# Kernel optimization log

Hardware: AMD Instinct MI355X
Metric: run time of the kernel (lower is better)

The kernel has to match this reference:

```python
import jax, jax.numpy as jnp
import numpy as np
from jax.scipy.special import logsumexp

PAD, SOS, EOS = 0, 2, 3
V, E, H, L, K = 30000, 128, 256, 2, 32   # vocab, embed, hidden, lstm layers, tags
B, T = 64, 512
HP = H // L                               # per-direction hidden size (PyTorch: hidden_sz//num_layer)


def setup_inputs() -> dict:
    key = jax.random.key(0)
    ks = jax.random.split(key, 20)
    # sorted-descending lengths (pack_padded_sequence requirement)
    lengths = jnp.sort(jax.random.randint(ks[0], (B,), T // 2, T + 1))[::-1]
    pos = jnp.arange(T)
    valid = pos[None, :] < lengths[:, None]
    x = jnp.where(valid, jax.random.randint(ks[1], (B, T), 4, V), PAD)
    y = jax.random.randint(ks[2], (B, T + 1), 4, K).at[:, 0].set(SOS)
    embed = jax.random.normal(ks[3], (V, E)) * 0.1
    s = 1.0 / np.sqrt(HP)
    u = lambda k, shape: jax.random.uniform(k, shape, minval=-s, maxval=s)
    p = {}
    i = 4
    for l, din in [(0, E), (1, 2 * HP)]:
        for d in 'fb':
            p['wi_l%d%s' % (l, d)] = u(ks[i], (4 * HP, din)); i += 1
            p['wh_l%d%s' % (l, d)] = u(ks[i], (4 * HP, HP)); i += 1
            p['b_l%d%s' % (l, d)] = u(ks[i], (4 * HP,)); i += 1
    so = 1.0 / np.sqrt(H)
    w_out = jax.random.uniform(ks[i], (K, H), minval=-so, maxval=so); i += 1
    b_out = jax.random.uniform(ks[i], (K,), minval=-so, maxval=so); i += 1
    trans = jax.random.normal(ks[i], (K, K))
    trans = trans.at[SOS, :].set(-10000.0)
    trans = trans.at[:, EOS].set(-10000.0)
    trans = trans.at[:, PAD].set(-10000.0)
    trans = trans.at[PAD, :].set(-10000.0)
    trans = trans.at[PAD, EOS].set(0.0)
    trans = trans.at[PAD, PAD].set(0.0)
    return {'x': x, 'y': y, 'embed': embed, **p, 'w_out': w_out, 'b_out': b_out, 'trans': trans}


def _lstm_dir(xs, wi, wh, b):
    # xs: [T, B, D] -> hidden states [T, B, HP]; PyTorch gate order i, f, g, o
    bsz = xs.shape[1]
    def step(carry, xt):
        h, c = carry
        z = xt @ wi.T + h @ wh.T + b
        i, f, g, o = jnp.split(z, 4, axis=-1)
        c = jax.nn.sigmoid(f) * c + jax.nn.sigmoid(i) * jnp.tanh(g)
        h = jax.nn.sigmoid(o) * jnp.tanh(c)
        return (h, c), h
    init = (jnp.zeros((bsz, HP), xs.dtype), jnp.zeros((bsz, HP), xs.dtype))
    _, hs = jax.lax.scan(step, init, xs)
    return hs


def _flip(a, lengths):
    # per-sequence reversal of valid prefix (matches packed-sequence reverse LSTM)
    pos = jnp.arange(a.shape[1])
    idx = jnp.where(pos[None, :] < lengths[:, None], lengths[:, None] - 1 - pos[None, :], pos[None, :])
    return jnp.take_along_axis(a, idx[:, :, None], axis=1)


def _bilstm_layer(inp, lengths, wif, whf, bf, wib, whb, bb):
    hf = _lstm_dir(inp.swapaxes(0, 1), wif, whf, bf).swapaxes(0, 1)
    hb = _flip(_lstm_dir(_flip(inp, lengths).swapaxes(0, 1), wib, whb, bb).swapaxes(0, 1), lengths)
    return jnp.concatenate([hf, hb], axis=-1)


def _forward(x, y, embed, wi_l0f, wh_l0f, b_l0f, wi_l0b, wh_l0b, b_l0b,
             wi_l1f, wh_l1f, b_l1f, wi_l1b, wh_l1b, b_l1b, w_out, b_out, trans):
    mask = (x > PAD).astype(jnp.float32)          # [B, T]
    lengths = mask.sum(1).astype(jnp.int32)       # [B]
    h = embed[x]                                  # [B, T, E]
    h = _bilstm_layer(h, lengths, wi_l0f, wh_l0f, b_l0f, wi_l0b, wh_l0b, b_l0b)
    h = _bilstm_layer(h, lengths, wi_l1f, wh_l1f, b_l1f, wi_l1b, wh_l1b, b_l1b)
    h = jnp.einsum('btd,kd->btk', h, w_out) + b_out   # emissions [B, T, K]
    h = h * mask[:, :, None]
    bsz = x.shape[0]
    # CRF partition function: sequential log-sum-exp recurrence
    init = jnp.full((bsz, K), -10000.0).at[:, SOS].set(0.0)
    def step(score, tb):
        h_t, m_t = tb                              # [B, K], [B]
        s = logsumexp(score[:, None, :] + h_t[:, :, None] + trans[None, :, :], axis=-1)
        return jnp.where(m_t[:, None] > 0, s, score), None
    score, _ = jax.lax.scan(step, init, (h.swapaxes(0, 1), mask.T))
    logZ = logsumexp(score + trans[EOS], axis=-1)
    # gold path score
    emit = jnp.take_along_axis(h, y[:, 1:, None], axis=2)[..., 0]  # [B, T]
    tr = trans[y[:, 1:], y[:, :-1]]                                 # [B, T]
    gold = ((emit + tr) * mask).sum(1)
    last_tag = jnp.take_along_axis(y, lengths[:, None], axis=1)[:, 0]
    gold = gold + trans[EOS, last_tag]
    return logZ - gold                              # [B] negative log-likelihood


def reference(x, y, embed, wi_l0f, wh_l0f, b_l0f, wi_l0b, wh_l0b, b_l0b,
              wi_l1f, wh_l1f, b_l1f, wi_l1b, wh_l1b, b_l1b, w_out, b_out, trans):
    return _forward(x, y, embed, wi_l0f, wh_l0f, b_l0f, wi_l0b, wh_l0b, b_l0b,
                    wi_l1f, wh_l1f, b_l1f, wi_l1b, wh_l1b, b_l1b, w_out, b_out, trans)
```

## Files before the change

### kernel.cpp

```cpp
#include <hip/hip_runtime.h>

typedef _Float16 half_t;
typedef _Float16 half2_t __attribute__((ext_vector_type(2)));
typedef _Float16 half4_t __attribute__((ext_vector_type(4)));
typedef _Float16 half8_t __attribute__((ext_vector_type(8)));
typedef float float4_t __attribute__((ext_vector_type(4)));

#define BB 64
#define TT 512
#define EE 128
#define HPP 128
#define KK 32
#define MTOT (BB*TT)
#define NWID 1024

__device__ __forceinline__ void lds_barrier() {
    asm volatile("s_waitcnt lgkmcnt(0)\n\ts_barrier" ::: "memory");
}

__device__ __forceinline__ float fast_sigmoid(float x) {
    return __builtin_amdgcn_rcpf(1.f + __expf(-x));
}
__device__ __forceinline__ float fast_tanh(float x) {
    return 1.f - 2.f * __builtin_amdgcn_rcpf(__expf(2.f * x) + 1.f);
}
__device__ __forceinline__ float readlane_f(float v, int lane) {
    return __builtin_bit_cast(float, __builtin_amdgcn_readlane(__builtin_bit_cast(int, v), lane));
}

__global__ void k_pack(const float* __restrict__ wi0f, const float* __restrict__ wi0b,
                       const float* __restrict__ wi1f, const float* __restrict__ wi1b,
                       const float* __restrict__ w_out,
                       const int* __restrict__ x, const float* __restrict__ embed,
                       half_t* __restrict__ WP0, half_t* __restrict__ WP1,
                       half_t* __restrict__ WO, half_t* __restrict__ e16,
                       int* __restrict__ lens) {
    if (blockIdx.x < BB) {
        __shared__ int cnt;
        if (threadIdx.x == 0) cnt = 0;
        __syncthreads();
        int local = 0;
        for (int t = threadIdx.x; t < TT; t += blockDim.x)
            local += (x[blockIdx.x * TT + t] > 0) ? 1 : 0;
        atomicAdd(&cnt, local);
        __syncthreads();
        if (threadIdx.x == 0) lens[blockIdx.x] = cnt;
    }

    int idx = blockIdx.x * blockDim.x + threadIdx.x;
    int stride = gridDim.x * blockDim.x;
    const int n0 = NWID * EE;
    const int n1 = NWID * 256;
    for (int i = idx; i < n0; i += stride) {
        int j8 = i & 7; int ln = (i >> 3) & 63; int rest = i >> 9;
        int kc = rest & 3; int ntg = rest >> 2;
        int lr = ln & 15, lq = ln >> 4;
        int n = ntg * 16 + lr;
        int k = kc * 32 + lq * 8 + j8;
        float v = (n < 512) ? wi0f[n * 128 + k] : wi0b[(n - 512) * 128 + k];
        WP0[i] = (half_t)v;
    }
    for (int i = idx; i < n1; i += stride) {
        int j8 = i & 7; int ln = (i >> 3) & 63; int rest = i >> 9;
        int kc = rest & 7; int ntg = rest >> 3;
        int lr = ln & 15, lq = ln >> 4;
        int n = ntg * 16 + lr;
        int k = kc * 32 + lq * 8 + j8;
        float v = (n < 512) ? wi1f[n * 256 + k] : wi1b[(n - 512) * 256 + k];
        WP1[i] = (half_t)v;
    }
    for (int i = idx; i < KK * 256; i += stride)
        WO[i] = (half_t)w_out[i];
    for (int i = idx; i < MTOT * 16; i += stride) {
        int bt = i >> 4;
        int c  = (i & 15) * 8;
        int xi = x[bt];
        const float4* src = (const float4*)(embed + (size_t)xi * EE + c);
        float4 a = src[0], b = src[1];
        half8_t o;
        o[0] = (half_t)a.x; o[1] = (half_t)a.y; o[2] = (half_t)a.z; o[3] = (half_t)a.w;
        o[4] = (half_t)b.x; o[5] = (half_t)b.y; o[6] = (half_t)b.z; o[7] = (half_t)b.w;
        *(half8_t*)(e16 + (size_t)bt * EE + c) = o;
    }
}

__global__ __launch_bounds__(256, 2) void k_gemm(const half_t* __restrict__ A,
                                                 const half_t* __restrict__ WP,
                                                 const float* __restrict__ bias_f,
                                                 const float* __restrict__ bias_b,
                                                 const int* __restrict__ lens,
                                                 half_t* __restrict__ C, int Kd) {
    {
        int t0 = (blockIdx.x * 128) & 511;
        if (t0 >= lens[blockIdx.x >> 2]) return;
    }
    const int KC = Kd >> 5;
    int wave = threadIdx.x >> 6;
    int lane = threadIdx.x & 63;
    int m0 = blockIdx.x * 128 + wave * 32;
    int dir = blockIdx.y >> 1;
    int cg  = blockIdx.y & 1;
    int lr = lane & 15;
    int lq = lane >> 4;

    float4_t acc0[16], acc1[16];
    #pragma unroll
    for (int i = 0; i < 16; i++) {
        acc0[i] = (float4_t){0.f, 0.f, 0.f, 0.f};
        acc1[i] = (float4_t){0.f, 0.f, 0.f, 0.f};
    }

    const half_t* Arow0 = A + (size_t)(m0 + lr) * Kd + lq * 8;
    const half_t* Arow1 = Arow0 + (size_t)16 * Kd;
    const int ntile0 = dir * 32 + cg * 4;
    const half_t* Wbase = WP + ((size_t)ntile0 * KC * 64 + lane) * 8;

    for (int kc = 0; kc < KC; kc++) {
        half8_t af0 = *(const half8_t*)(Arow0 + kc * 32);
        half8_t af1 = *(const half8_t*)(Arow1 + kc * 32);
        #pragma unroll
        for (int nt = 0; nt < 16; nt++) {
            int g = nt >> 2, sub = nt & 3;
            half8_t bf = *(const half8_t*)(Wbase + (((size_t)(g * 8 + sub) * KC + kc) << 9));
            acc0[nt] = __builtin_amdgcn_mfma_f32_16x16x32_f16(af0, bf, acc0[nt], 0, 0, 0);
            acc1[nt] = __builtin_amdgcn_mfma_f32_16x16x32_f16(af1, bf, acc1[nt], 0, 0, 0);
        }
    }

    const float* bias = dir ? bias_b : bias_f;
    char* Crow = (char*)C + dir * 1024 + (size_t)(cg * 64) * 8;
    #pragma unroll
    for (int sub = 0; sub < 4; sub++) {
        int cbase = cg * 64 + sub * 16 + lr;
        float b0 = bias[cbase];
        float b1 = bias[128 + cbase];
        float b2 = bias[256 + cbase];
        float b3 = bias[384 + cbase];
        #pragma unroll
        for (int i = 0; i < 4; i++) {
            int m = m0 + lq * 4 + i;
            half4_t o;
            o[0] = (half_t)(acc0[0 * 4 + sub][i] + b0);
            o[1] = (half_t)(acc0[1 * 4 + sub][i] + b1);
            o[2] = (half_t)(acc0[2 * 4 + sub][i] + b2);
            o[3] = (half_t)(acc0[3 * 4 + sub][i] + b3);
            *(half4_t*)(Crow + (size_t)m * 2048 + (sub * 16 + lr) * 8) = o;
            half4_t o2;
            o2[0] = (half_t)(acc1[0 * 4 + sub][i] + b0);
            o2[1] = (half_t)(acc1[1 * 4 + sub][i] + b1);
            o2[2] = (half_t)(acc1[2 * 4 + sub][i] + b2);
            o2[3] = (half_t)(acc1[3 * 4 + sub][i] + b3);
            *(half4_t*)(Crow + (size_t)(m + 16) * 2048 + (sub * 16 + lr) * 8) = o2;
        }
    }
}

__global__ __launch_bounds__(512, 1) void k_lstm(const half_t* __restrict__ zbuf,
                                                 const float* __restrict__ wh_f,
                                                 const float* __restrict__ wh_b,
                                                 const int* __restrict__ lens,
                                                 half_t* __restrict__ hout) {
    const int grp  = blockIdx.x >> 1;
    const int dir  = blockIdx.x & 1;
    const int tid  = threadIdx.x;
    const int wv   = tid >> 6;
    const int lane = tid & 63;
    const int q    = lane >> 4;
    const int col  = lane & 15;
    const int s    = col & 3;
    const int ii   = col >> 2;
    const int b    = grp * 4 + s;
    const int Lb   = lens[b];
    const int maxL = lens[grp * 4];
    const float* wh = dir ? wh_b : wh_f;

    __shared__ half_t hb[2][512];

    half8_t a0[4], a1[4], a2[4], a3[4];
    #pragma unroll
    for (int i = 0; i < 4; i++) {
        int r = wv * 64 + i * 16 + col;
        int orow = (r & 3) * 128 + (r >> 2);
        #pragma unroll
        for (int ck = 0; ck < 4; ck++) {
            const float4* src = (const float4*)(wh + (size_t)orow * 128 + ck * 32 + q * 8);
            float4 f0 = src[0], f1 = src[1];
            half8_t h8;
            h8[0] = (half_t)f0.x; h8[1] = (half_t)f0.y; h8[2] = (half_t)f0.z; h8[3] = (half_t)f0.w;
            h8[4] = (half_t)f1.x; h8[5] = (half_t)f1.y; h8[6] = (half_t)f1.z; h8[7] = (half_t)f1.w;
            if (i == 0) a0[ck] = h8;
            else if (i == 1) a1[ck] = h8;
            else if (i == 2) a2[ck] = h8;
            else a3[ck] = h8;
        }
    }

    hb[0][tid] = (half_t)0.f;

    const int cell = wv * 16 + ii * 4 + q;
    const int woff = (cell >> 5) * 128 + (s * 4 + ((cell >> 3) & 3)) * 8 + (cell & 7);
    const int roff = (s * 4 + q) * 8;

    const bool s1 = (ii == 1), s2 = (ii == 2), s3 = (ii == 3);

    float c = 0.f;
    const char* zb8  = (const char*)zbuf + dir * 1024;
    char*       hob8 = (char*)hout + dir * 256;

    const int zdelta = dir ? -2048 : 2048;
    const int hdelta = dir ? -512 : 512;

    int t0 = dir ? (Lb - 1) : 0;
    int t1 = dir ? (Lb - 2) : 1;
    half4_t z1 = *(const half4_t*)(zb8 + (unsigned)((b * TT + t0) * 2048 + cell * 8));
    half4_t z2 = *(const half4_t*)(zb8 + (unsigned)((b * TT + t1) * 2048 + cell * 8));

    int zoff = (b * TT + (dir ? (Lb - 3) : 2)) * 2048 + cell * 8;
    int hoff = (b * TT + t0) * 512 + cell * 2;
    const unsigned deadoff = (unsigned)((b * TT + 511) * 512 + cell * 2);

    __syncthreads();

    const int maxL2 = (maxL + 1) & ~1;

#define LSTM_STEP(RB, ZC, T)                                                      \
    {                                                                             \
        half8_t bf0 = *(const half8_t*)&hb[RB][roff];                             \
        half8_t bf1 = *(const half8_t*)&hb[RB][128 + roff];                       \
        half8_t bf2 = *(const half8_t*)&hb[RB][256 + roff];                       \
        half8_t bf3 = *(const half8_t*)&hb[RB][384 + roff];                       \
        float4_t A0 = (float4_t){0.f, 0.f, 0.f, 0.f};                             \
        float4_t A1 = (float4_t){0.f, 0.f, 0.f, 0.f};                             \
        float4_t A2 = (float4_t){0.f, 0.f, 0.f, 0.f};                             \
        float4_t A3 = (float4_t){0.f, 0.f, 0.f, 0.f};                             \
        A0 = __builtin_amdgcn_mfma_f32_16x16x32_f16(a0[0], bf0, A0, 0, 0, 0);     \
        A1 = __builtin_amdgcn_mfma_f32_16x16x32_f16(a1[0], bf0, A1, 0, 0, 0);     \
        A2 = __builtin_amdgcn_mfma_f32_16x16x32_f16(a2[0], bf0, A2, 0, 0, 0);     \
        A3 = __builtin_amdgcn_mfma_f32_16x16x32_f16(a3[0], bf0, A3, 0, 0, 0);     \
        A0 = __builtin_amdgcn_mfma_f32_16x16x32_f16(a0[1], bf1, A0, 0, 0, 0);     \
        A1 = __builtin_amdgcn_mfma_f32_16x16x32_f16(a1[1], bf1, A1, 0, 0, 0);     \
        A2 = __builtin_amdgcn_mfma_f32_16x16x32_f16(a2[1], bf1, A2, 0, 0, 0);     \
        A3 = __builtin_amdgcn_mfma_f32_16x16x32_f16(a3[1], bf1, A3, 0, 0, 0);     \
        A0 = __builtin_amdgcn_mfma_f32_16x16x32_f16(a0[2], bf2, A0, 0, 0, 0);     \
        A1 = __builtin_amdgcn_mfma_f32_16x16x32_f16(a1[2], bf2, A1, 0, 0, 0);     \
        A2 = __builtin_amdgcn_mfma_f32_16x16x32_f16(a2[2], bf2, A2, 0, 0, 0);     \
        A3 = __builtin_amdgcn_mfma_f32_16x16x32_f16(a3[2], bf2, A3, 0, 0, 0);     \
        A0 = __builtin_amdgcn_mfma_f32_16x16x32_f16(a0[3], bf3, A0, 0, 0, 0);     \
        A1 = __builtin_amdgcn_mfma_f32_16x16x32_f16(a1[3], bf3, A1, 0, 0, 0);     \
        A2 = __builtin_amdgcn_mfma_f32_16x16x32_f16(a2[3], bf3, A2, 0, 0, 0);     \
        A3 = __builtin_amdgcn_mfma_f32_16x16x32_f16(a3[3], bf3, A3, 0, 0, 0);     \
        float g0 = s1 ? A1[0] : (s2 ? A2[0] : (s3 ? A3[0] : A0[0]));              \
        float g1 = s1 ? A1[1] : (s2 ? A2[1] : (s3 ? A3[1] : A0[1]));              \
        float g2 = s1 ? A1[2] : (s2 ? A2[2] : (s3 ? A3[2] : A0[2]));              \
        float g3 = s1 ? A1[3] : (s2 ? A2[3] : (s3 ? A3[3] : A0[3]));              \
        float zi = g0 + (float)ZC[0];                                             \
        float zf = g1 + (float)ZC[1];                                             \
        float zg = g2 + (float)ZC[2];                                             \
        float zo = g3 + (float)ZC[3];                                             \
        ZC = *(const half4_t*)(zb8 + (unsigned)zoff);         \
        zoff += zdelta;                                                           \
        zoff = zoff < 0 ? 0 : zoff;                                               \
        float si = fast_sigmoid(zi);                                              \
        float sf = fast_sigmoid(zf);                                              \
        float so = fast_sigmoid(zo);                                              \
        float tg = fast_tanh(zg);                                                 \
        c = sf * c + si * tg;                                                     \
        float th = fast_tanh(c);                                                  \
        half_t hh = (half_t)(so * th);                                            \
        hb[RB ^ 1][woff] = hh;                                                    \
        unsigned soff = ((T) < Lb) ? (unsigned)hoff : deadoff;                    \
        *(half_t*)(hob8 + soff) = hh;                        \
        hoff += hdelta;                                                           \
        lds_barrier();                                                            \
    }

    for (int t = 0; t < maxL2; t += 2) {
        LSTM_STEP(0, z1, t)
        LSTM_STEP(1, z2, t + 1)
    }
#undef LSTM_STEP
}

__global__ __launch_bounds__(256) void k_logits(const half_t* __restrict__ h1,
                                                const half_t* __restrict__ WO,
                                                const float* __restrict__ b_out,
                                                const int* __restrict__ lens,
                                                float* __restrict__ logits) {
    {
        int t0 = (blockIdx.x * 64) & 511;
        if (t0 >= lens[blockIdx.x >> 3]) return;
    }
    int wave = threadIdx.x >> 6;
    int lane = threadIdx.x & 63;
    int m0 = blockIdx.x * 64 + wave * 16;
    int lr = lane & 15;
    int lq = lane >> 4;

    float4_t acc0 = (float4_t){0.f, 0.f, 0.f, 0.f};
    float4_t acc1 = (float4_t){0.f, 0.f, 0.f, 0.f};

    const half_t* Arow = h1 + (size_t)(m0 + lr) * 256 + lq * 8;
    const half_t* Brow = WO + (size_t)lr * 256 + lq * 8;

    #pragma unroll
    for (int k = 0; k < 256; k += 32) {
        half8_t af = *(const half8_t*)(Arow + k);
        half8_t b0 = *(const half8_t*)(Brow + k);
        half8_t b1 = *(const half8_t*)(Brow + 16 * 256 + k);
        acc0 = __builtin_amdgcn_mfma_f32_16x16x32_f16(af, b0, acc0, 0, 0, 0);
        acc1 = __builtin_amdgcn_mfma_f32_16x16x32_f16(af, b1, acc1, 0, 0, 0);
    }
    #pragma unroll
    for (int nt = 0; nt < 2; nt++) {
        int n = nt * 16 + lr;
        float bias = b_out[n];
        #pragma unroll
        for (int i = 0; i < 4; i++) {
            int m = m0 + lq * 4 + i;
            logits[(size_t)m * KK + n] = (nt == 0 ? acc0[i] : acc1[i]) + bias;
        }
    }
}

__global__ __launch_bounds__(64) void k_crf(const float* __restrict__ logits,
                                            const float* __restrict__ trans,
                                            const int* __restrict__ y,
                                            const int* __restrict__ lens,
                                            float* __restrict__ out) {
    int b = blockIdx.x;
    int lane = threadIdx.x;
    int k = lane & 31;
    __shared__ float TR[32][33];

    for (int i = lane; i < 1024; i += 64) TR[i >> 5][i & 31] = trans[i];

    float et[32];
    const float* trow = trans + k * 32;
    #pragma unroll
    for (int j = 0; j < 32; j++) et[j] = __expf(trow[j]);
    __syncthreads();

    int Lb = lens[b];
    const int* yb = y + b * (TT + 1);
    const float* lgb = logits + (size_t)(b * TT) * KK;

    float g = 0.f;
    for (int t = lane; t < Lb; t += 64) {
        int yt = yb[t], yt1 = yb[t + 1];
        g += lgb[(size_t)t * KK + yt1] + TR[yt1][yt];
    }
    #pragma unroll
    for (int s = 1; s < 64; s <<= 1) g += __shfl_xor(g, s);
    float gold = g + TR[3][yb[Lb]];

    float score = lgb[k] + TR[k][2];

    const float* lgp = lgb + KK + k;
    float lg_cur = *lgp;
    for (int t = 1; t < Lb; t++) {
        float lg_use = lg_cur;
        lgp += KK;
        lg_cur = *lgp;
        float m = readlane_f(score, 4);
        float P = __expf(score - m);
        float a0 = 0.f, a1 = 0.f, a2 = 0.f, a3 = 0.f;
        #pragma unroll
        for (int j = 0; j < 8; j++) {
            a0 = fmaf(et[j],      readlane_f(P, j),      a0);
            a1 = fmaf(et[j + 8],  readlane_f(P, j + 8),  a1);
            a2 = fmaf(et[j + 16], readlane_f(P, j + 16), a2);
            a3 = fmaf(et[j + 24], readlane_f(P, j + 24), a3);
        }
        score = lg_use + m + __logf((a0 + a1) + (a2 + a3));
    }

    float v = score + TR[3][k];
    float m2 = v;
    #pragma unroll
    for (int s = 1; s < 32; s <<= 1) m2 = fmaxf(m2, __shfl_xor(m2, s));
    float e = __expf(v - m2);
    #pragma unroll
    for (int s = 1; s < 32; s <<= 1) e += __shfl_xor(e, s);
    float logZ = m2 + __logf(e);

    if (lane == 0) out[b] = logZ - gold;
}

extern "C" void kernel_launch(void* const* d_in, const int* in_sizes, int n_in,
                              void* d_out, int out_size, void* d_ws, size_t ws_size,
                              hipStream_t stream) {
    const int*   x      = (const int*)d_in[0];
    const int*   y      = (const int*)d_in[1];
    const float* embed  = (const float*)d_in[2];
    const float* wi_l0f = (const float*)d_in[3];
    const float* wh_l0f = (const float*)d_in[4];
    const float* b_l0f  = (const float*)d_in[5];
    const float* wi_l0b = (const float*)d_in[6];
    const float* wh_l0b = (const float*)d_in[7];
    const float* b_l0b  = (const float*)d_in[8];
    const float* wi_l1f = (const float*)d_in[9];
    const float* wh_l1f = (const float*)d_in[10];
    const float* b_l1f  = (const float*)d_in[11];
    const float* wi_l1b = (const float*)d_in[12];
    const float* wh_l1b = (const float*)d_in[13];
    const float* b_l1b  = (const float*)d_in[14];
    const float* w_out  = (const float*)d_in[15];
    const float* b_out  = (const float*)d_in[16];
    const float* trans  = (const float*)d_in[17];
    float* out = (float*)d_out;

    char* base = (char*)d_ws;
    size_t off = 0;
    auto take = [&](size_t bytes) -> char* {
        char* r = base + off;
        off = (off + bytes + 255) & ~(size_t)255;
        return r;
    };
    half_t* zA  = (half_t*)take((size_t)MTOT * NWID * 2);
    half_t* h0  = (half_t*)take((size_t)MTOT * 256 * 2);
    half_t* h1  = (half_t*)take((size_t)MTOT * 256 * 2);
    half_t* e16 = (half_t*)take((size_t)MTOT * EE * 2);
    float*  lg  = (float*)take((size_t)MTOT * KK * 4);
    half_t* WP0 = (half_t*)take((size_t)NWID * EE * 2);
    half_t* WP1 = (half_t*)take((size_t)NWID * 256 * 2);
    half_t* WO  = (half_t*)take((size_t)KK * 256 * 2);
    int*    lens = (int*)take(BB * 4);

    k_pack<<<512, 256, 0, stream>>>(wi_l0f, wi_l0b, wi_l1f, wi_l1b, w_out, x, embed,
                                    WP0, WP1, WO, e16, lens);
    k_gemm<<<dim3(MTOT / 128, 4), 256, 0, stream>>>(e16, WP0, b_l0f, b_l0b, lens, zA, 128);
    k_lstm<<<32, 512, 0, stream>>>(zA, wh_l0f, wh_l0b, lens, h0);
    k_gemm<<<dim3(MTOT / 128, 4), 256, 0, stream>>>(h0, WP1, b_l1f, b_l1b, lens, zA, 256);
    k_lstm<<<32, 512, 0, stream>>>(zA, wh_l1f, wh_l1b, lens, h1);
    k_logits<<<MTOT / 64, 256, 0, stream>>>(h1, WO, b_out, lens, lg);
    k_crf<<<BB, 64, 0, stream>>>(lg, trans, y, lens, out);
}
```

Before: 844.0 us.

## Fuse output logits projection into CRF kernel with LDS-resident half logits

```diff
diff --git a/kernel.cpp b/kernel.cpp
--- a/kernel.cpp
+++ b/kernel.cpp
@@ -281,86 +281,84 @@
 #undef LSTM_STEP
 }
 
-__global__ __launch_bounds__(256) void k_logits(const half_t* __restrict__ h1,
-                                                const half_t* __restrict__ WO,
-                                                const float* __restrict__ b_out,
-                                                const int* __restrict__ lens,
-                                                float* __restrict__ logits) {
-    {
-        int t0 = (blockIdx.x * 64) & 511;
-        if (t0 >= lens[blockIdx.x >> 3]) return;
-    }
-    int wave = threadIdx.x >> 6;
-    int lane = threadIdx.x & 63;
-    int m0 = blockIdx.x * 64 + wave * 16;
-    int lr = lane & 15;
-    int lq = lane >> 4;
-
-    float4_t acc0 = (float4_t){0.f, 0.f, 0.f, 0.f};
-    float4_t acc1 = (float4_t){0.f, 0.f, 0.f, 0.f};
-
-    const half_t* Arow = h1 + (size_t)(m0 + lr) * 256 + lq * 8;
-    const half_t* Brow = WO + (size_t)lr * 256 + lq * 8;
-
-    #pragma unroll
-    for (int k = 0; k < 256; k += 32) {
-        half8_t af = *(const half8_t*)(Arow + k);
-        half8_t b0 = *(const half8_t*)(Brow + k);
-        half8_t b1 = *(const half8_t*)(Brow + 16 * 256 + k);
-        acc0 = __builtin_amdgcn_mfma_f32_16x16x32_f16(af, b0, acc0, 0, 0, 0);
-        acc1 = __builtin_amdgcn_mfma_f32_16x16x32_f16(af, b1, acc1, 0, 0, 0);
-    }
-    #pragma unroll
-    for (int nt = 0; nt < 2; nt++) {
-        int n = nt * 16 + lr;
-        float bias = b_out[n];
+__global__ __launch_bounds__(256) void k_crf(const half_t* __restrict__ h1,
+                                             const half_t* __restrict__ WO,
+                                             const float* __restrict__ b_out,
+                                             const float* __restrict__ trans,
+                                             const int* __restrict__ y,
+                                             const int* __restrict__ lens,
+                                             float* __restrict__ out) {
+    const int b = blockIdx.x;
+    const int tid = threadIdx.x;
+    const int wv = tid >> 6;
+    const int lane = tid & 63;
+    const int lr = lane & 15;
+    const int lq = lane >> 4;
+    const int Lb = lens[b];
+
+    __shared__ half_t LG[TT * KK];
+    __shared__ float TR[32][33];
+    __shared__ float gpart[4];
+
+    for (int i = tid; i < 1024; i += 256) TR[i >> 5][i & 31] = trans[i];
+
+    half8_t bf[2][8];
+    #pragma unroll
+    for (int nt = 0; nt < 2; nt++)
+        #pragma unroll
+        for (int kc = 0; kc < 8; kc++)
+            bf[nt][kc] = *(const half8_t*)(WO + (size_t)(nt * 16 + lr) * 256 + kc * 32 + lq * 8);
+    float bias0 = b_out[lr];
+    float bias1 = b_out[16 + lr];
+
+    const int ntiles = (Lb + 15) >> 4;
+    for (int tile = wv; tile < ntiles; tile += 4) {
+        const half_t* Arow = h1 + (size_t)(b * TT + tile * 16 + lr) * 256 + lq * 8;
+        float4_t acc0 = (float4_t){0.f, 0.f, 0.f, 0.f};
+        float4_t acc1 = (float4_t){0.f, 0.f, 0.f, 0.f};
+        #pragma unroll
+        for (int kc = 0; kc < 8; kc++) {
+            half8_t af = *(const half8_t*)(Arow + kc * 32);
+            acc0 = __builtin_amdgcn_mfma_f32_16x16x32_f16(af, bf[0][kc], acc0, 0, 0, 0);
+            acc1 = __builtin_amdgcn_mfma_f32_16x16x32_f16(af, bf[1][kc], acc1, 0, 0, 0);
+        }
         #pragma unroll
         for (int i = 0; i < 4; i++) {
-            int m = m0 + lq * 4 + i;
-            logits[(size_t)m * KK + n] = (nt == 0 ? acc0[i] : acc1[i]) + bias;
-        }
-    }
-}
-
-__global__ __launch_bounds__(64) void k_crf(const float* __restrict__ logits,
-                                            const float* __restrict__ trans,
-                                            const int* __restrict__ y,
-                                            const int* __restrict__ lens,
-                                            float* __restrict__ out) {
-    int b = blockIdx.x;
-    int lane = threadIdx.x;
-    int k = lane & 31;
-    __shared__ float TR[32][33];
-
-    for (int i = lane; i < 1024; i += 64) TR[i >> 5][i & 31] = trans[i];
+            int t = tile * 16 + lq * 4 + i;
+            LG[t * KK + lr]      = (half_t)(acc0[i] + bias0);
+            LG[t * KK + 16 + lr] = (half_t)(acc1[i] + bias1);
+        }
+    }
+    __syncthreads();
+
+    const int* yb = y + b * (TT + 1);
+    float g = 0.f;
+    for (int t = tid; t < Lb; t += 256) {
+        int yt = yb[t], yt1 = yb[t + 1];
+        g += (float)LG[t * KK + yt1] + TR[yt1][yt];
+    }
+    #pragma unroll
+    for (int s = 1; s < 64; s <<= 1) g += __shfl_xor(g, s);
+    if (lane == 0) gpart[wv] = g;
+    __syncthreads();
+
+    if (wv != 0) return;
+
+    const int k = lane & 31;
+    float gold = gpart[0] + gpart[1] + gpart[2] + gpart[3] + TR[3][yb[Lb]];
 
     float et[32];
     const float* trow = trans + k * 32;
     #pragma unroll
     for (int j = 0; j < 32; j++) et[j] = __expf(trow[j]);
-    __syncthreads();
-
-    int Lb = lens[b];
-    const int* yb = y + b * (TT + 1);
-    const float* lgb = logits + (size_t)(b * TT) * KK;
-
-    float g = 0.f;
-    for (int t = lane; t < Lb; t += 64) {
-        int yt = yb[t], yt1 = yb[t + 1];
-        g += lgb[(size_t)t * KK + yt1] + TR[yt1][yt];
-    }
-    #pragma unroll
-    for (int s = 1; s < 64; s <<= 1) g += __shfl_xor(g, s);
-    float gold = g + TR[3][yb[Lb]];
-
-    float score = lgb[k] + TR[k][2];
-
-    const float* lgp = lgb + KK + k;
-    float lg_cur = *lgp;
+
+    float score = (float)LG[k] + TR[k][2];
+
+    float lg_cur = (float)LG[KK + k];
     for (int t = 1; t < Lb; t++) {
         float lg_use = lg_cur;
-        lgp += KK;
-        lg_cur = *lgp;
+        int tn = (t + 1 < TT) ? (t + 1) : t;
+        lg_cur = (float)LG[tn * KK + k];
         float m = readlane_f(score, 4);
         float P = __expf(score - m);
         float a0 = 0.f, a1 = 0.f, a2 = 0.f, a3 = 0.f;
@@ -420,7 +418,6 @@
     half_t* h0  = (half_t*)take((size_t)MTOT * 256 * 2);
     half_t* h1  = (half_t*)take((size_t)MTOT * 256 * 2);
     half_t* e16 = (half_t*)take((size_t)MTOT * EE * 2);
-    float*  lg  = (float*)take((size_t)MTOT * KK * 4);
     half_t* WP0 = (half_t*)take((size_t)NWID * EE * 2);
     half_t* WP1 = (half_t*)take((size_t)NWID * 256 * 2);
     half_t* WO  = (half_t*)take((size_t)KK * 256 * 2);
@@ -432,6 +429,5 @@
     k_lstm<<<32, 512, 0, stream>>>(zA, wh_l0f, wh_l0b, lens, h0);
     k_gemm<<<dim3(MTOT / 128, 4), 256, 0, stream>>>(h0, WP1, b_l1f, b_l1b, lens, zA, 256);
     k_lstm<<<32, 512, 0, stream>>>(zA, wh_l1f, wh_l1b, lens, h1);
-    k_logits<<<MTOT / 64, 256, 0, stream>>>(h1, WO, b_out, lens, lg);
-    k_crf<<<BB, 64, 0, stream>>>(lg, trans, y, lens, out);
-}
+    k_crf<<<BB, 256, 0, stream>>>(h1, WO, b_out, trans, y, lens, out);
+}
```

Result: no change. 858.2 us (+1.7%).
